# Kernel optimization log

Hardware: AMD Instinct MI355X
Metric: run time of the kernel (lower is better)

Reference implementation:

```python
import jax, jax.numpy as jnp
import numpy as np

TOP_K = 2


def setup_inputs() -> dict:
    key = jax.random.key(0)
    ks = jax.random.split(key, 5)
    B, S, D, F, E = 2, 2048, 1024, 3584, 8
    scale_in = 1.0 / np.sqrt(D)
    scale_f = 1.0 / np.sqrt(F)
    return {
        "hidden_states": jax.random.normal(ks[0], (B, S, D), dtype=jnp.float32),
        "gate_w": jax.random.normal(ks[1], (E, D), dtype=jnp.float32) * scale_in,
        "w1": jax.random.normal(ks[2], (E, F, D), dtype=jnp.float32) * scale_in,
        "w3": jax.random.normal(ks[3], (E, F, D), dtype=jnp.float32) * scale_in,
        "w2": jax.random.normal(ks[4], (E, D, F), dtype=jnp.float32) * scale_f,
    }


def _routing_weights(logits):
    # softmax over experts, select top-k, renormalize (Mixtral semantics)
    probs = jax.nn.softmax(logits, axis=-1)          # [T, E]
    topv, topi = jax.lax.top_k(probs, TOP_K)          # [T, k]
    topv = topv / jnp.sum(topv, axis=-1, keepdims=True)
    T, E = logits.shape
    w = jnp.zeros((T, E), dtype=logits.dtype)
    w = w.at[jnp.arange(T)[:, None], topi].set(topv)  # dense [T, E] routing weights
    return w


def reference(hidden_states, gate_w, w1, w3, w2):
    B, S, D = hidden_states.shape
    x = hidden_states.reshape(-1, D)                  # [T, D]
    logits = x @ gate_w.T                             # [T, E]
    rw = _routing_weights(logits)                     # [T, E]
    E = gate_w.shape[0]
    out = jnp.zeros_like(x)
    for e in range(E):                                # fixed small expert count
        h = jax.nn.silu(x @ w1[e].T) * (x @ w3[e].T)  # [T, F]
        out = out + rw[:, e:e + 1] * (h @ w2[e].T)    # [T, D]
    return out.reshape(B, S, D)
```

## Files before the change

kernel.cpp:

```cpp
#include <hip/hip_runtime.h>
#include <hip/hip_bf16.h>


#define T_TOK 4096
#define DIM   1024
#define FF    3584
#define NE    8
#define CAP   (T_TOK*2 + NE*256)

#define OFF_TOPI   256UL
#define OFF_TOPW   33024UL
#define OFF_ROWTOK 65792UL
#define OFF_ROWW   106752UL
#define OFF_W1B    147712UL
#define OFF_W3B    (OFF_W1B + 58720256UL)
#define OFF_W2B    OFF_W1B
#define OFF_H      (OFF_W1B + 117440512UL)
#define WS_NEED    (OFF_H + 73400320UL)

using f32x4 = __attribute__((ext_vector_type(4))) float;
using s16x8 = __attribute__((ext_vector_type(8))) short;

__device__ __forceinline__ ushort f2b(float f) {
    __hip_bfloat16 b = __float2bfloat16(f);
    ushort u; __builtin_memcpy(&u, &b, 2); return u;
}
__device__ __forceinline__ void gl_lds16(const ushort* g, ushort* l) {
    __builtin_amdgcn_global_load_lds(
        (const __attribute__((address_space(1))) void*)g,
        (__attribute__((address_space(3))) void*)l, 16, 0, 0);
}
__device__ __forceinline__ uint4 pack8(float4 v0, float4 v1) {
    uint4 o;
    o.x = f2b(v0.x) | ((uint)f2b(v0.y) << 16);
    o.y = f2b(v0.z) | ((uint)f2b(v0.w) << 16);
    o.z = f2b(v1.x) | ((uint)f2b(v1.y) << 16);
    o.w = f2b(v1.z) | ((uint)f2b(v1.w) << 16);
    return o;
}

#define LGKM0 do { asm volatile("s_waitcnt lgkmcnt(0)" ::: "memory"); \
                   __builtin_amdgcn_sched_barrier(0); } while (0)
#define VMC(n) asm volatile("s_waitcnt vmcnt(" #n ")" ::: "memory")
#define BAR()  __builtin_amdgcn_s_barrier()

__global__ __launch_bounds__(256)
void k_route(const float* __restrict__ x, const float* __restrict__ gw,
             int* __restrict__ topi, float* __restrict__ topw,
             int* __restrict__ counts, ushort* __restrict__ xb)
{
    __shared__ float gws[NE*DIM];
    const int tid = threadIdx.x;
    for (int i = tid; i < NE*DIM/4; i += 256)
        ((float4*)gws)[i] = ((const float4*)gw)[i];
    __syncthreads();

    const int lane = tid & 63, wid = tid >> 6;
    const int t = blockIdx.x*4 + wid;

    float4 xr[4];
    const float4* xrow = (const float4*)(x + (size_t)t*DIM) + lane*4;
    #pragma unroll
    for (int i = 0; i < 4; ++i) xr[i] = xrow[i];

    uint4* xbd = (uint4*)(xb + (size_t)t*DIM);
    xbd[lane*2]   = pack8(xr[0], xr[1]);
    xbd[lane*2+1] = pack8(xr[2], xr[3]);

    float lg[NE];
    #pragma unroll
    for (int e = 0; e < NE; ++e) {
        const float4* g4 = (const float4*)(gws + e*DIM) + lane*4;
        float s = 0.f;
        #pragma unroll
        for (int i = 0; i < 4; ++i) {
            float4 g = g4[i];
            s += xr[i].x*g.x + xr[i].y*g.y + xr[i].z*g.z + xr[i].w*g.w;
        }
        #pragma unroll
        for (int off = 32; off; off >>= 1) s += __shfl_xor(s, off);
        lg[e] = s;
    }
    if (lane == 0) {
        float b1 = -1e30f, b2 = -1e30f; int i1 = 0, i2 = 0;
        #pragma unroll
        for (int e = 0; e < NE; ++e) {
            float v = lg[e];
            if (v > b1)      { b2 = b1; i2 = i1; b1 = v; i1 = e; }
            else if (v > b2) { b2 = v; i2 = e; }
        }
        float p2 = __expf(b2 - b1);
        float inv = 1.f / (1.f + p2);
        topi[2*t]   = i1; topi[2*t+1] = i2;
        topw[2*t]   = inv; topw[2*t+1] = p2*inv;
        atomicAdd(&counts[i1], 1); atomicAdd(&counts[i2], 1);
    }
}

__global__ void k_scan(const int* __restrict__ counts, int* __restrict__ offs,
                       int* __restrict__ rowTok)
{
    if (threadIdx.x == 0) {
        int acc = 0; offs[0] = 0;
        for (int e = 0; e < NE; ++e) {
            int p = (counts[e] + 255) & ~255;
            acc += p; offs[e+1] = acc;
        }
    }
    for (int i = threadIdx.x; i < CAP; i += blockDim.x) rowTok[i] = -1;
}

__global__ __launch_bounds__(256)
void k_scatter(const int* __restrict__ topi, const float* __restrict__ topw,
               const int* __restrict__ offs, int* __restrict__ cursor,
               int* __restrict__ rowTok, float* __restrict__ rowW)
{
    int t = blockIdx.x*256 + threadIdx.x;
    #pragma unroll
    for (int j = 0; j < 2; ++j) {
        int e = topi[2*t + j];
        int pos = offs[e] + atomicAdd(&cursor[e], 1);
        rowTok[pos] = t;
        rowW[pos] = topw[2*t + j];
    }
}

__global__ __launch_bounds__(256)
void k_cvt(const float* __restrict__ src, ushort* __restrict__ dst)
{
    size_t i = (size_t)blockIdx.x*256 + threadIdx.x;
    float4 v0 = ((const float4*)src)[2*i], v1 = ((const float4*)src)[2*i+1];
    ((uint4*)dst)[i] = pack8(v0, v1);
}

#define G1_SLOT 12288
__global__ __launch_bounds__(256, 2)
void k_gemm1(const ushort* __restrict__ xb,
             const ushort* __restrict__ w1b, const ushort* __restrict__ w3b,
             const int* __restrict__ offs, const int* __restrict__ rowTok,
             ushort* __restrict__ hout)
{
    __shared__ __align__(16) ushort L[3*G1_SLOT];
    const int sb = blockIdx.x;
    const int rowStart = blockIdx.y * 256;
    if (rowStart >= offs[8]) return;
    int e = 0;
    #pragma unroll
    for (int k = 1; k < NE; ++k) if (rowStart >= offs[k]) e = k;

    const int tid = threadIdx.x, lane = tid & 63, wid = tid >> 6;
    const int wr = wid >> 1, wc = wid & 1;
    const int lo = lane & 15, hi = lane >> 4;

    const int srow = lane >> 2;
    const int sch  = (lane & 3) ^ ((lane >> 3) & 3);
    const ushort* aS[4];
    #pragma unroll
    for (int j = 0; j < 4; ++j) {
        int tk = rowTok[rowStart + j*64 + wid*16 + srow]; if (tk < 0) tk = 0;
        aS[j] = xb + (size_t)tk*DIM + sch*8;
    }
    const ushort* bS[2];
    bS[0] = w1b + ((size_t)e*FF + sb*64 + wid*16 + srow)*DIM + sch*8;
    bS[1] = w3b + ((size_t)e*FF + sb*64 + wid*16 + srow)*DIM + sch*8;
    ushort* const dA = L + wid*512;
    ushort* const dB = L + 8192 + wid*512;

    const int sig = (lo >> 1) & 3;
    const int roff = ((hi ^ sig) * 8);
    int rdA[8], rdB[4];
    #pragma unroll
    for (int m = 0; m < 8; ++m) rdA[m] = (wr*128 + m*16 + lo)*32 + roff;
    #pragma unroll
    for (int n = 0; n < 2; ++n) {
        rdB[n]   = 8192 + (wc*32 + n*16 + lo)*32 + roff;
        rdB[n+2] = 8192 + (64 + wc*32 + n*16 + lo)*32 + roff;
    }

    f32x4 acc[8][4];
    #pragma unroll
    for (int m = 0; m < 8; ++m)
        #pragma unroll
        for (int n = 0; n < 4; ++n) acc[m][n] = (f32x4)(0.f);

    #pragma unroll
    for (int t0 = 0; t0 < 2; ++t0) {
        #pragma unroll
        for (int j = 0; j < 4; ++j) gl_lds16(aS[j] + t0*32, dA + t0*G1_SLOT + j*2048);
        #pragma unroll
        for (int j = 0; j < 2; ++j) gl_lds16(bS[j] + t0*32, dB + t0*G1_SLOT + j*2048);
    }
    VMC(6);
    BAR();

    const int NK = DIM/32;
    int cur = 0, nxt = 2;
    for (int t = 0; t < NK; ++t) {
        const ushort* Lb = L + cur*G1_SLOT;
        const bool pf = (t + 2 < NK);
        s16x8 a[4], b[4];
        #pragma unroll
        for (int n = 0; n < 4; ++n) b[n] = *(const s16x8*)(Lb + rdB[n]);
        #pragma unroll
        for (int m = 0; m < 4; ++m) a[m] = *(const s16x8*)(Lb + rdA[m]);
        if (pf) {
            #pragma unroll
            for (int j = 0; j < 3; ++j)
                gl_lds16(aS[j] + (t+2)*32, dA + nxt*G1_SLOT + j*2048);
        }
        BAR();
        LGKM0;
        __builtin_amdgcn_s_setprio(1);
        #pragma unroll
        for (int m = 0; m < 4; ++m)
            #pragma unroll
            for (int n = 0; n < 4; ++n)
                acc[m][n] = __builtin_amdgcn_mfma_f32_16x16x32_bf16(a[m], b[n], acc[m][n], 0, 0, 0);
        __builtin_amdgcn_s_setprio(0);
        BAR();
        #pragma unroll
        for (int m = 0; m < 4; ++m) a[m] = *(const s16x8*)(Lb + rdA[4+m]);
        if (pf) {
            gl_lds16(aS[3] + (t+2)*32, dA + nxt*G1_SLOT + 3*2048);
            gl_lds16(bS[0] + (t+2)*32, dB + nxt*G1_SLOT);
            gl_lds16(bS[1] + (t+2)*32, dB + nxt*G1_SLOT + 2048);
        }
        BAR();
        LGKM0;
        __builtin_amdgcn_s_setprio(1);
        #pragma unroll
        for (int m = 0; m < 4; ++m)
            #pragma unroll
            for (int n = 0; n < 4; ++n)
                acc[4+m][n] = __builtin_amdgcn_mfma_f32_16x16x32_bf16(a[m], b[n], acc[4+m][n], 0, 0, 0);
        __builtin_amdgcn_s_setprio(0);
        if (t < NK-2) { VMC(6); } else { VMC(0); }
        BAR();
        cur = (cur == 2) ? 0 : cur + 1;
        nxt = (nxt == 2) ? 0 : nxt + 1;
    }

    #pragma unroll
    for (int m = 0; m < 8; ++m)
        #pragma unroll
        for (int p = 0; p < 2; ++p) {
            f32x4 v1 = acc[m][p], v3 = acc[m][p+2];
            int f = sb*64 + wc*32 + p*16 + lo;
            #pragma unroll
            for (int j = 0; j < 4; ++j) {
                int row = rowStart + wr*128 + m*16 + hi*4 + j;
                float s = v1[j];
                float val = (s / (1.f + __expf(-s))) * v3[j];
                hout[(size_t)row*FF + f] = f2b(val);
            }
        }
}

__global__ __launch_bounds__(256, 2)
void k_gemm2(const ushort* __restrict__ h, const ushort* __restrict__ w2b,
             const int* __restrict__ offs, const int* __restrict__ rowTok,
             const float* __restrict__ rowW, float* __restrict__ out)
{
    __shared__ __align__(16) ushort L[3*G1_SLOT];
    const int dc = blockIdx.x * 128;
    const int rowStart = blockIdx.y * 256;
    if (rowStart >= offs[8]) return;
    int e = 0;
    #pragma unroll
    for (int k = 1; k < NE; ++k) if (rowStart >= offs[k]) e = k;
    const int kbase = blockIdx.z * (FF/2);

    const int tid = threadIdx.x, lane = tid & 63, wid = tid >> 6;
    const int wr = wid >> 1, wc = wid & 1;
    const int lo = lane & 15, hi = lane >> 4;

    const int srow = lane >> 2;
    const int sch  = (lane & 3) ^ ((lane >> 3) & 3);
    const ushort* aS[4];
    #pragma unroll
    for (int j = 0; j < 4; ++j)
        aS[j] = h + (size_t)(rowStart + j*64 + wid*16 + srow)*FF + kbase + sch*8;
    const ushort* bS[2];
    #pragma unroll
    for (int j = 0; j < 2; ++j)
        bS[j] = w2b + ((size_t)e*DIM + dc + j*64 + wid*16 + srow)*FF + kbase + sch*8;
    ushort* const dA = L + wid*512;
    ushort* const dB = L + 8192 + wid*512;

    const int sig = (lo >> 1) & 3;
    const int roff = ((hi ^ sig) * 8);
    int rdA[8], rdB[4];
    #pragma unroll
    for (int m = 0; m < 8; ++m) rdA[m] = (wr*128 + m*16 + lo)*32 + roff;
    #pragma unroll
    for (int n = 0; n < 4; ++n) rdB[n] = 8192 + (wc*64 + n*16 + lo)*32 + roff;

    f32x4 acc[8][4];
    #pragma unroll
    for (int m = 0; m < 8; ++m)
        #pragma unroll
        for (int n = 0; n < 4; ++n) acc[m][n] = (f32x4)(0.f);

    #pragma unroll
    for (int t0 = 0; t0 < 2; ++t0) {
        #pragma unroll
        for (int j = 0; j < 4; ++j) gl_lds16(aS[j] + t0*32, dA + t0*G1_SLOT + j*2048);
        #pragma unroll
        for (int j = 0; j < 2; ++j) gl_lds16(bS[j] + t0*32, dB + t0*G1_SLOT + j*2048);
    }
    VMC(6);
    BAR();

    const int NK = (FF/2)/32;
    int cur = 0, nxt = 2;
    for (int t = 0; t < NK; ++t) {
        const ushort* Lb = L + cur*G1_SLOT;
        const bool pf = (t + 2 < NK);
        s16x8 a[4], b[4];
        #pragma unroll
        for (int n = 0; n < 4; ++n) b[n] = *(const s16x8*)(Lb + rdB[n]);
        #pragma unroll
        for (int m = 0; m < 4; ++m) a[m] = *(const s16x8*)(Lb + rdA[m]);
        if (pf) {
            #pragma unroll
            for (int j = 0; j < 3; ++j)
                gl_lds16(aS[j] + (t+2)*32, dA + nxt*G1_SLOT + j*2048);
        }
        BAR();
        LGKM0;
        __builtin_amdgcn_s_setprio(1);
        #pragma unroll
        for (int m = 0; m < 4; ++m)
            #pragma unroll
            for (int n = 0; n < 4; ++n)
                acc[m][n] = __builtin_amdgcn_mfma_f32_16x16x32_bf16(a[m], b[n], acc[m][n], 0, 0, 0);
        __builtin_amdgcn_s_setprio(0);
        BAR();
        #pragma unroll
        for (int m = 0; m < 4; ++m) a[m] = *(const s16x8*)(Lb + rdA[4+m]);
        if (pf) {
            gl_lds16(aS[3] + (t+2)*32, dA + nxt*G1_SLOT + 3*2048);
            gl_lds16(bS[0] + (t+2)*32, dB + nxt*G1_SLOT);
            gl_lds16(bS[1] + (t+2)*32, dB + nxt*G1_SLOT + 2048);
        }
        BAR();
        LGKM0;
        __builtin_amdgcn_s_setprio(1);
        #pragma unroll
        for (int m = 0; m < 4; ++m)
            #pragma unroll
            for (int n = 0; n < 4; ++n)
                acc[4+m][n] = __builtin_amdgcn_mfma_f32_16x16x32_bf16(a[m], b[n], acc[4+m][n], 0, 0, 0);
        __builtin_amdgcn_s_setprio(0);
        if (t < NK-2) { VMC(6); } else { VMC(0); }
        BAR();
        cur = (cur == 2) ? 0 : cur + 1;
        nxt = (nxt == 2) ? 0 : nxt + 1;
    }

    #pragma unroll
    for (int m = 0; m < 8; ++m)
        #pragma unroll
        for (int j = 0; j < 4; ++j) {
            int prow = rowStart + wr*128 + m*16 + hi*4 + j;
            int tok = rowTok[prow];
            if (tok < 0) continue;
            float w = rowW[prow];
            #pragma unroll
            for (int n = 0; n < 4; ++n) {
                int d = dc + wc*64 + n*16 + lo;
                atomicAdd(&out[(size_t)tok*DIM + d], w * acc[m][n][j]);
            }
        }
}

extern "C" void kernel_launch(void* const* d_in, const int* in_sizes, int n_in,
                              void* d_out, int out_size, void* d_ws, size_t ws_size,
                              hipStream_t stream)
{
    const float* x  = (const float*)d_in[0];
    const float* gw = (const float*)d_in[1];
    const float* w1 = (const float*)d_in[2];
    const float* w3 = (const float*)d_in[3];
    const float* w2 = (const float*)d_in[4];
    float* out = (float*)d_out;
    char* ws = (char*)d_ws;
    if (ws_size < WS_NEED) return;

    int*    counts = (int*)ws;
    int*    cursor = counts + 8;
    int*    offs   = counts + 16;
    int*    topi   = (int*)  (ws + OFF_TOPI);
    float*  topw   = (float*)(ws + OFF_TOPW);
    int*    rowTok = (int*)  (ws + OFF_ROWTOK);
    float*  rowW   = (float*)(ws + OFF_ROWW);
    ushort* w1b    = (ushort*)(ws + OFF_W1B);
    ushort* w3b    = (ushort*)(ws + OFF_W3B);
    ushort* w2b    = (ushort*)(ws + OFF_W2B);
    ushort* h      = (ushort*)(ws + OFF_H);
    ushort* xb     = (ushort*)d_out;

    hipMemsetAsync(ws, 0, 256, stream);

    k_route  <<<T_TOK/4, 256, 0, stream>>>(x, gw, topi, topw, counts, xb);
    k_scan   <<<1, 256, 0, stream>>>(counts, offs, rowTok);
    k_scatter<<<T_TOK/256, 256, 0, stream>>>(topi, topw, offs, cursor, rowTok, rowW);
    k_cvt    <<<(NE*FF*DIM/8)/256, 256, 0, stream>>>(w1, w1b);
    k_cvt    <<<(NE*FF*DIM/8)/256, 256, 0, stream>>>(w3, w3b);
    k_gemm1  <<<dim3(56, CAP/256), 256, 0, stream>>>(xb, w1b, w3b, offs, rowTok, h);
    k_cvt    <<<(NE*DIM*FF/8)/256, 256, 0, stream>>>(w2, w2b);
    hipMemsetAsync(d_out, 0, (size_t)T_TOK*DIM*4, stream);
    k_gemm2  <<<dim3(8, CAP/256, 2), 256, 0, stream>>>(h, w2b, offs, rowTok, rowW, out);
}
```

Before: 533.9 us.

## Use double-buffered LDS pipeline in gemm2 and merge w1/w3 conversion launches

The down-projection GEMM kernel moves from a three-slot LDS ring with split prefetch and fine-grained vmcnt waits to a simple two-slot double buffer. Each iteration prefetches the whole next tile and ends with one __syncthreads. The smaller LDS footprint and a raised launch bound of 3 blocks per CU are meant to raise occupancy. The trade-off is less latency hiding per block and higher register pressure, which could cause spills. Separately, the two fp32-to-bf16 weight conversions for w1 and w3 are fused into a single kernel launch to cut launch overhead.

```diff
diff --git a/kernel.cpp b/kernel.cpp
--- a/kernel.cpp
+++ b/kernel.cpp
@@ -133,6 +133,20 @@
     ((uint4*)dst)[i] = pack8(v0, v1);
 }
 
+#define CVT_HALF ((NE*FF*DIM/8)/256)
+__global__ __launch_bounds__(256)
+void k_cvt2(const float* __restrict__ w1, const float* __restrict__ w3,
+            ushort* __restrict__ w1b, ushort* __restrict__ w3b)
+{
+    int b = blockIdx.x;
+    const float* src; ushort* dst;
+    if (b < CVT_HALF) { src = w1; dst = w1b; }
+    else              { src = w3; dst = w3b; b -= CVT_HALF; }
+    size_t i = (size_t)b*256 + threadIdx.x;
+    float4 v0 = ((const float4*)src)[2*i], v1 = ((const float4*)src)[2*i+1];
+    ((uint4*)dst)[i] = pack8(v0, v1);
+}
+
 #define G1_SLOT 12288
 __global__ __launch_bounds__(256, 2)
 void k_gemm1(const ushort* __restrict__ xb,
@@ -256,12 +270,13 @@
         }
 }
 
-__global__ __launch_bounds__(256, 2)
+#define G2_SLOT 12288
+__global__ __launch_bounds__(256, 3)
 void k_gemm2(const ushort* __restrict__ h, const ushort* __restrict__ w2b,
              const int* __restrict__ offs, const int* __restrict__ rowTok,
              const float* __restrict__ rowW, float* __restrict__ out)
 {
-    __shared__ __align__(16) ushort L[3*G1_SLOT];
+    __shared__ __align__(16) ushort L[2*G2_SLOT];
     const int dc = blockIdx.x * 128;
     const int rowStart = blockIdx.y * 256;
     if (rowStart >= offs[8]) return;
@@ -302,32 +317,28 @@
         for (int n = 0; n < 4; ++n) acc[m][n] = (f32x4)(0.f);
 
     #pragma unroll
-    for (int t0 = 0; t0 < 2; ++t0) {
-        #pragma unroll
-        for (int j = 0; j < 4; ++j) gl_lds16(aS[j] + t0*32, dA + t0*G1_SLOT + j*2048);
-        #pragma unroll
-        for (int j = 0; j < 2; ++j) gl_lds16(bS[j] + t0*32, dB + t0*G1_SLOT + j*2048);
-    }
-    VMC(6);
-    BAR();
+    for (int j = 0; j < 4; ++j) gl_lds16(aS[j], dA + j*2048);
+    #pragma unroll
+    for (int j = 0; j < 2; ++j) gl_lds16(bS[j], dB + j*2048);
+    __syncthreads();
 
     const int NK = (FF/2)/32;
-    int cur = 0, nxt = 2;
+    int cur = 0;
     for (int t = 0; t < NK; ++t) {
-        const ushort* Lb = L + cur*G1_SLOT;
-        const bool pf = (t + 2 < NK);
+        const ushort* Lb = L + cur*G2_SLOT;
+        if (t + 1 < NK) {
+            ushort* Ln = L + (cur ^ 1)*G2_SLOT;
+            const int o = (t + 1)*32;
+            #pragma unroll
+            for (int j = 0; j < 4; ++j) gl_lds16(aS[j] + o, Ln + wid*512 + j*2048);
+            #pragma unroll
+            for (int j = 0; j < 2; ++j) gl_lds16(bS[j] + o, Ln + 8192 + wid*512 + j*2048);
+        }
         s16x8 a[4], b[4];
         #pragma unroll
         for (int n = 0; n < 4; ++n) b[n] = *(const s16x8*)(Lb + rdB[n]);
         #pragma unroll
         for (int m = 0; m < 4; ++m) a[m] = *(const s16x8*)(Lb + rdA[m]);
-        if (pf) {
-            #pragma unroll
-            for (int j = 0; j < 3; ++j)
-                gl_lds16(aS[j] + (t+2)*32, dA + nxt*G1_SLOT + j*2048);
-        }
-        BAR();
-        LGKM0;
         __builtin_amdgcn_s_setprio(1);
         #pragma unroll
         for (int m = 0; m < 4; ++m)
@@ -335,16 +346,8 @@
             for (int n = 0; n < 4; ++n)
                 acc[m][n] = __builtin_amdgcn_mfma_f32_16x16x32_bf16(a[m], b[n], acc[m][n], 0, 0, 0);
         __builtin_amdgcn_s_setprio(0);
-        BAR();
         #pragma unroll
         for (int m = 0; m < 4; ++m) a[m] = *(const s16x8*)(Lb + rdA[4+m]);
-        if (pf) {
-            gl_lds16(aS[3] + (t+2)*32, dA + nxt*G1_SLOT + 3*2048);
-            gl_lds16(bS[0] + (t+2)*32, dB + nxt*G1_SLOT);
-            gl_lds16(bS[1] + (t+2)*32, dB + nxt*G1_SLOT + 2048);
-        }
-        BAR();
-        LGKM0;
         __builtin_amdgcn_s_setprio(1);
         #pragma unroll
         for (int m = 0; m < 4; ++m)
@@ -352,10 +355,8 @@
             for (int n = 0; n < 4; ++n)
                 acc[4+m][n] = __builtin_amdgcn_mfma_f32_16x16x32_bf16(a[m], b[n], acc[4+m][n], 0, 0, 0);
         __builtin_amdgcn_s_setprio(0);
-        if (t < NK-2) { VMC(6); } else { VMC(0); }
-        BAR();
-        cur = (cur == 2) ? 0 : cur + 1;
-        nxt = (nxt == 2) ? 0 : nxt + 1;
+        __syncthreads();
+        cur ^= 1;
     }
 
     #pragma unroll
@@ -405,8 +406,7 @@
     k_route  <<<T_TOK/4, 256, 0, stream>>>(x, gw, topi, topw, counts, xb);
     k_scan   <<<1, 256, 0, stream>>>(counts, offs, rowTok);
     k_scatter<<<T_TOK/256, 256, 0, stream>>>(topi, topw, offs, cursor, rowTok, rowW);
-    k_cvt    <<<(NE*FF*DIM/8)/256, 256, 0, stream>>>(w1, w1b);
-    k_cvt    <<<(NE*FF*DIM/8)/256, 256, 0, stream>>>(w3, w3b);
+    k_cvt2   <<<2*CVT_HALF, 256, 0, stream>>>(w1, w3, w1b, w3b);
     k_gemm1  <<<dim3(56, CAP/256), 256, 0, stream>>>(xb, w1b, w3b, offs, rowTok, h);
     k_cvt    <<<(NE*DIM*FF/8)/256, 256, 0, stream>>>(w2, w2b);
     hipMemsetAsync(d_out, 0, (size_t)T_TOK*DIM*4, stream);
```

After: 565.0 us. 5.8% more time.
